# Kernel optimization log

Hardware: AMD Instinct MI355X
Metric: run time of the kernel (lower is better)

## Reference

```python
import jax, jax.numpy as jnp
import numpy as np

B, T, E, H, C = 64, 256, 1024, 1024, 32000


def setup_inputs() -> dict:
    key = jax.random.key(0)
    ks = jax.random.split(key, 8)
    s = 0.02
    return {
        "X": jax.random.randint(ks[0], (B, T), 0, C),
        "emb": jax.random.normal(ks[1], (C, E), jnp.float32) * s,
        "Wi1": jax.random.normal(ks[2], (4, H, E), jnp.float32) * s,
        "Wh1": jax.random.normal(ks[3], (4, H, H), jnp.float32) * s,
        "bi1": jnp.ones((4, H), jnp.float32),
        "bh1": jnp.ones((4, H), jnp.float32),
        "Wi2": jax.random.normal(ks[4], (4, H, E), jnp.float32) * s,
        "Wh2": jax.random.normal(ks[5], (4, H, H), jnp.float32) * s,
        "bi2": jnp.ones((4, H), jnp.float32),
        "bh2": jnp.ones((4, H), jnp.float32),
        "W": jax.random.normal(ks[6], (C, H), jnp.float32) * s,
        "b": jnp.ones((C,), jnp.float32),
    }


def _lstm_last_o(x_tbe, Wi, Wh, bi, bh):
    """Run LSTM over time; return the LAST output gate o_T, shape [B, H].

    x_tbe: [T, B, E]; Wi: [4, H, E]; Wh: [4, H, H]; bi, bh: [4, H]
    Gate order g = 0:i, 1:f, 2:g(cell cand), 3:o. Original module adds BOTH
    biases (b_i_* + b_h_*) every step.
    """
    Tn, Bn = x_tbe.shape[0], x_tbe.shape[1]
    Hn = Wh.shape[1]
    # Precompute input projections for all timesteps: [T, B, 4, H]
    xp = jnp.einsum('tbe,ghe->tbgh', x_tbe, Wi) + bi + bh

    def step(carry, xp_t):
        h, c, _ = carry
        g = xp_t + jnp.einsum('bh,gkh->bgk', h, Wh)  # [B, 4, H]
        i_t = jax.nn.sigmoid(g[:, 0])
        f_t = jax.nn.sigmoid(g[:, 1])
        g_t = jnp.tanh(g[:, 2])
        o_t = jax.nn.sigmoid(g[:, 3])
        c_new = f_t * c + i_t * g_t
        h_new = o_t * jnp.tanh(c_new)
        return (h_new, c_new, o_t), None

    z = jnp.zeros((Bn, Hn), x_tbe.dtype)
    (h_f, c_f, o_f), _ = jax.lax.scan(step, (z, z, z), xp)
    return o_f


def reference(X, emb, Wi1, Wh1, bi1, bh1, Wi2, Wh2, bi2, bh2, W, b):
    x = emb[X]                     # [B, T, E]
    xt = jnp.transpose(x, (1, 0, 2))  # [T, B, E]
    o1 = _lstm_last_o(xt, Wi1, Wh1, bi1, bh1)           # forward direction
    o2 = _lstm_last_o(xt[::-1], Wi2, Wh2, bi2, bh2)     # reversed direction
    return (o1 + o2) @ W.T + b      # [B, n_class]
```

## Files before the change

### kernel.cpp

```cpp
#include <hip/hip_runtime.h>
#include <hip/hip_bf16.h>
#include <stdint.h>

typedef __attribute__((ext_vector_type(4))) float    f32x4;
typedef __attribute__((ext_vector_type(8))) short    bf16x8;
typedef __attribute__((ext_vector_type(4))) uint32_t u32x4;
typedef unsigned short u16;

#define T_   256
#define B_   64
#define E_   1024
#define H_   1024
#define CLS  32000
#define NWG  256

#define OFF_XBF   0ull
#define OFF_WHP   33554432ull
#define OFF_FLG   67108864ull
#define OFF_BSUM  67141632ull
#define OFF_OBUF  67174400ull
#define OFF_OSUM  67698688ull
#define OFF_HROT  67829760ull

__device__ __forceinline__ u16 f2bf(float f) {
    union { float f; uint32_t i; } v; v.f = f;
    uint32_t r = v.i + 0x7fffu + ((v.i >> 16) & 1u);
    return (u16)(r >> 16);
}
__device__ __forceinline__ float sigm(float x)   { return 1.f / (1.f + __expf(-x)); }
__device__ __forceinline__ float tanh_f(float x) { return 1.f - 2.f / (__expf(2.f * x) + 1.f); }

__device__ __forceinline__ void ldg4_cc(unsigned& d, const unsigned* p) {
    asm volatile("global_load_dword %0, %1, off sc0 sc1"
                 : "=v"(d) : "v"(p) : "memory");
}
__device__ __forceinline__ void stg16_cc(u16* p, bf16x8 v) {
    asm volatile("global_store_dwordx4 %0, %1, off sc0 sc1"
                 :: "v"(p), "v"(v) : "memory");
}
__device__ __forceinline__ void stg4_cc(unsigned* p, unsigned v) {
    asm volatile("global_store_dword %0, %1, off sc0 sc1"
                 :: "v"(p), "v"(v) : "memory");
}
__device__ __forceinline__ void wait_vm0() {
    asm volatile("s_waitcnt vmcnt(0)" ::: "memory");
}


__global__ void k_gather(const int* __restrict__ X, const float* __restrict__ emb,
                         u16* __restrict__ xbf) {
    const int m = blockIdx.x;
    const int t = m >> 6, b = m & 63;
    const int tok = X[b * T_ + t];
    const float* src = emb + (size_t)tok * E_;
    u16* dst = xbf + (size_t)m * E_;
    const int e = threadIdx.x * 4;
    float4 v = *(const float4*)(src + e);
    ushort4 o; o.x = f2bf(v.x); o.y = f2bf(v.y); o.z = f2bf(v.z); o.w = f2bf(v.w);
    *(ushort4*)(dst + e) = o;
}

__global__ void k_packw(const float* __restrict__ Wi1, const float* __restrict__ Wh1,
                        const float* __restrict__ Wi2, const float* __restrict__ Wh2,
                        u16* __restrict__ whp) {
    const int gi  = blockIdx.x * 256 + threadIdx.x;
    const int half = gi >> 20;
    const int r   = gi & 1048575;
    const int wg  = r >> 12;
    const int lin = r & 4095;
    const int kc  = lin & 127;
    const int col = lin >> 7;
    const int dir = wg >> 7, hblk = wg & 127;
    const int g = col >> 3, hh = col & 7;
    const float* W = half ? (dir ? Wh2 : Wh1) : (dir ? Wi2 : Wi1);
    const float* src = W + (size_t)(g * H_ + hblk * 8 + hh) * H_ + kc * 8;
    float4 v0 = *(const float4*)(src);
    float4 v1 = *(const float4*)(src + 4);
    const uint32_t boff = (uint32_t)(((kc * 32 + col) * 16) ^ ((kc & 3) << 4));
    u16* dst = whp + (size_t)wg * 65536 + half * 32768 + boff / 2;
    ushort4 o0, o1;
    o0.x = f2bf(v0.x); o0.y = f2bf(v0.y); o0.z = f2bf(v0.z); o0.w = f2bf(v0.w);
    o1.x = f2bf(v1.x); o1.y = f2bf(v1.y); o1.z = f2bf(v1.z); o1.w = f2bf(v1.w);
    *(ushort4*)dst = o0;
    *(ushort4*)(dst + 4) = o1;
}

__global__ void k_bias(const float* __restrict__ bi1, const float* __restrict__ bh1,
                       const float* __restrict__ bi2, const float* __restrict__ bh2,
                       float* __restrict__ bsum) {
    const int i = blockIdx.x * 256 + threadIdx.x;
    bsum[i] = (i < 4096) ? (bi1[i] + bh1[i]) : (bi2[i - 4096] + bh2[i - 4096]);
}

__global__ __launch_bounds__(512, 1) void k_lstm(
    const u16* __restrict__ xbf, const u16* __restrict__ whp,
    const float* __restrict__ bsum, u16* hrot,
    float* __restrict__ obuf, unsigned* cnt) {
    __shared__ __align__(16) u16 wlds[65536];
    __shared__ float glds[2][64][35];
    __shared__ __align__(16) u16 hxch[64][8];
    const int wg = blockIdx.x;
    const int dir = wg >> 7, hblk = wg & 127;
    const int tid = threadIdx.x;
    const int wid = tid >> 6, lane = tid & 63;
    const int mtile = wid & 3, khalf = wid >> 2;
    const int col16 = lane & 15, kslot = lane >> 4;
    {
        const u32x4* s = (const u32x4*)(whp + (size_t)wg * 65536);
        u32x4* d = (u32x4*)wlds;
#pragma unroll
        for (int i = 0; i < 16; ++i) d[tid + i * 512] = s[tid + i * 512];
    }
    const int fb = tid >> 3, fh = tid & 7;
    const int hidx = hblk * 8 + fh;
    const int arow = mtile * 16 + col16;
    float bsF[4];
#pragma unroll
    for (int g = 0; g < 4; ++g) bsF[g] = bsum[dir * 4096 + g * 1024 + hidx];
    const unsigned* pollp = cnt + (size_t)(dir * 128 + khalf * 64 + lane) * 32;
    unsigned* flag_own = cnt + (size_t)(dir * 128 + hblk) * 32;
    float cc = 0.f;
    __syncthreads();
    for (int s = 0; s < T_; ++s) {
        const int t = dir ? (T_ - 1 - s) : s;
        const u16* xrow = xbf + (size_t)(t * 64 + arow) * 1024 + khalf * 512;
        bf16x8 xa[16];
#pragma unroll
        for (int kk = 0; kk < 16; ++kk)
            xa[kk] = *(const bf16x8*)(xrow + kk * 32 + kslot * 8);
        if (s > 0) {
            const unsigned target = (unsigned)s;
            for (;;) {
                unsigned f;
                ldg4_cc(f, pollp);
                wait_vm0();
                if (__all(f >= target)) break;
                __builtin_amdgcn_s_sleep(1);
            }
        }
        __builtin_amdgcn_sched_barrier(0);
        const u16* hbase = hrot + (size_t)(s * 2 + dir) * 131072
                         + (size_t)(khalf * 64) * 512 + arow * 8;
        bf16x8 hf[16];
#pragma unroll
        for (int kk = 0; kk < 16; ++kk)
            hf[kk] = *(const bf16x8*)(hbase + (size_t)(kk * 4 + kslot) * 512);
        f32x4 acc0 = {0.f, 0.f, 0.f, 0.f}, acc1 = {0.f, 0.f, 0.f, 0.f};
#pragma unroll
        for (int kk = 0; kk < 16; ++kk) {
            const int kc = khalf * 64 + kk * 4 + kslot;
            const uint32_t base = (uint32_t)(kc * 512);
            const uint32_t sw = (uint32_t)((kc & 3) << 4);
            bf16x8 b0 = *(const bf16x8*)((const char*)wlds + ((base + (uint32_t)(col16 * 16)) ^ sw));
            bf16x8 b1 = *(const bf16x8*)((const char*)wlds + ((base + (uint32_t)(256 + col16 * 16)) ^ sw));
            acc0 = __builtin_amdgcn_mfma_f32_16x16x32_bf16(xa[kk], b0, acc0, 0, 0, 0);
            acc1 = __builtin_amdgcn_mfma_f32_16x16x32_bf16(xa[kk], b1, acc1, 0, 0, 0);
        }
#pragma unroll
        for (int kk = 0; kk < 16; ++kk) {
            const int kc = khalf * 64 + kk * 4 + kslot;
            const uint32_t base = (uint32_t)(65536 + kc * 512);
            const uint32_t sw = (uint32_t)((kc & 3) << 4);
            bf16x8 b0 = *(const bf16x8*)((const char*)wlds + ((base + (uint32_t)(col16 * 16)) ^ sw));
            bf16x8 b1 = *(const bf16x8*)((const char*)wlds + ((base + (uint32_t)(256 + col16 * 16)) ^ sw));
            acc0 = __builtin_amdgcn_mfma_f32_16x16x32_bf16(hf[kk], b0, acc0, 0, 0, 0);
            acc1 = __builtin_amdgcn_mfma_f32_16x16x32_bf16(hf[kk], b1, acc1, 0, 0, 0);
        }
#pragma unroll
        for (int q = 0; q < 4; ++q) {
            glds[khalf][mtile * 16 + kslot * 4 + q][col16]      = acc0[q];
            glds[khalf][mtile * 16 + kslot * 4 + q][16 + col16] = acc1[q];
        }
        __syncthreads();
        const float gi = glds[0][fb][fh]      + glds[1][fb][fh]      + bsF[0];
        const float gf = glds[0][fb][8 + fh]  + glds[1][fb][8 + fh]  + bsF[1];
        const float gc = glds[0][fb][16 + fh] + glds[1][fb][16 + fh] + bsF[2];
        const float go = glds[0][fb][24 + fh] + glds[1][fb][24 + fh] + bsF[3];
        const float iv = sigm(gi), fv = sigm(gf), gv = tanh_f(gc), ov = sigm(go);
        cc = fv * cc + iv * gv;
        const float hv = ov * tanh_f(cc);
        hxch[fb][fh] = f2bf(hv);
        if (s == T_ - 1) obuf[(size_t)(dir * 64 + fb) * 1024 + hidx] = ov;
        __syncthreads();
        if (wid == 0) {
            bf16x8 hv8 = *(const bf16x8*)(&hxch[lane][0]);
            u16* hst = hrot + (size_t)((s + 1) * 2 + dir) * 131072
                     + (size_t)hblk * 512 + lane * 8;
            stg16_cc(hst, hv8);
            wait_vm0();
            if (lane == 0) stg4_cc(flag_own, (unsigned)(s + 1));
        }
    }
}


__global__ void k_osum(const float* __restrict__ obuf, u16* __restrict__ osum) {
    const int i = blockIdx.x * 256 + threadIdx.x;
    osum[i] = f2bf(obuf[i] + obuf[65536 + i]);
}

__global__ __launch_bounds__(256) void k_cls(const u16* __restrict__ osum,
                                             const float* __restrict__ W,
                                             const float* __restrict__ bias,
                                             float* __restrict__ out) {
    const int blk = blockIdx.x;
    const int tid = threadIdx.x, wid = tid >> 6, lane = tid & 63;
    const int col16 = lane & 15, kslot = lane >> 4;
    const int ncol0 = blk * 128 + wid * 32;
    f32x4 acc[4][2] = {};
    for (int kk = 0; kk < 32; ++kk) {
        const int kof = kk * 32 + kslot * 8;
        bf16x8 a[4];
#pragma unroll
        for (int mi = 0; mi < 4; ++mi)
            a[mi] = *(const bf16x8*)(osum + (mi * 16 + col16) * 1024 + kof);
#pragma unroll
        for (int nt = 0; nt < 2; ++nt) {
            const float* wr = W + (size_t)(ncol0 + nt * 16 + col16) * 1024 + kof;
            float4 w0 = *(const float4*)wr;
            float4 w1 = *(const float4*)(wr + 4);
            union { bf16x8 v; u16 u[8]; } bb;
            bb.u[0] = f2bf(w0.x); bb.u[1] = f2bf(w0.y); bb.u[2] = f2bf(w0.z); bb.u[3] = f2bf(w0.w);
            bb.u[4] = f2bf(w1.x); bb.u[5] = f2bf(w1.y); bb.u[6] = f2bf(w1.z); bb.u[7] = f2bf(w1.w);
#pragma unroll
            for (int mi = 0; mi < 4; ++mi)
                acc[mi][nt] = __builtin_amdgcn_mfma_f32_16x16x32_bf16(a[mi], bb.v, acc[mi][nt], 0, 0, 0);
        }
    }
#pragma unroll
    for (int nt = 0; nt < 2; ++nt) {
        const int cn = ncol0 + nt * 16 + col16;
        const float bv = bias[cn];
#pragma unroll
        for (int mi = 0; mi < 4; ++mi)
#pragma unroll
            for (int q = 0; q < 4; ++q)
                out[(size_t)(mi * 16 + kslot * 4 + q) * CLS + cn] = acc[mi][nt][q] + bv;
    }
}


extern "C" void kernel_launch(void* const* d_in, const int* in_sizes, int n_in,
                              void* d_out, int out_size, void* d_ws, size_t ws_size,
                              hipStream_t stream) {
    const int*   X   = (const int*)d_in[0];
    const float* emb = (const float*)d_in[1];
    const float* Wi1 = (const float*)d_in[2];
    const float* Wh1 = (const float*)d_in[3];
    const float* bi1 = (const float*)d_in[4];
    const float* bh1 = (const float*)d_in[5];
    const float* Wi2 = (const float*)d_in[6];
    const float* Wh2 = (const float*)d_in[7];
    const float* bi2 = (const float*)d_in[8];
    const float* bh2 = (const float*)d_in[9];
    const float* W   = (const float*)d_in[10];
    const float* bb  = (const float*)d_in[11];
    float* out = (float*)d_out;
    char* ws = (char*)d_ws;

    u16*      xbf   = (u16*)(ws + OFF_XBF);
    u16*      whp   = (u16*)(ws + OFF_WHP);
    unsigned* cnt   = (unsigned*)(ws + OFF_FLG);
    float*    bsum  = (float*)(ws + OFF_BSUM);
    float*    obuf  = (float*)(ws + OFF_OBUF);
    u16*      osum  = (u16*)(ws + OFF_OSUM);
    u16*      hrot  = (u16*)(ws + OFF_HROT);

    k_gather<<<dim3(16384), dim3(256), 0, stream>>>(X, emb, xbf);
    k_packw<<<dim3(8192), dim3(256), 0, stream>>>(Wi1, Wh1, Wi2, Wh2, whp);
    k_bias<<<dim3(32), dim3(256), 0, stream>>>(bi1, bh1, bi2, bh2, bsum);
    hipMemsetAsync(hrot, 0, 262144, stream);
    hipMemsetAsync(cnt, 0, 32768, stream);
    {
        const u16* xb_p = xbf; const u16* whp_p = whp; const float* bs_p = bsum;
        u16* hr_p = hrot; float* ob_p = obuf; unsigned* cnt_p = cnt;
        void* args[] = { (void*)&xb_p, (void*)&whp_p, (void*)&bs_p,
                         (void*)&hr_p, (void*)&ob_p, (void*)&cnt_p };
        hipError_t e = hipLaunchCooperativeKernel((void*)k_lstm, dim3(NWG), dim3(512),
                                                  args, 0, stream);
        if (e != hipSuccess) {
            k_lstm<<<dim3(NWG), dim3(512), 0, stream>>>(xbf, whp, bsum, hrot, obuf, cnt);
        }
    }
    k_osum<<<dim3(256), dim3(256), 0, stream>>>(obuf, osum);
    k_cls<<<dim3(250), dim3(256), 0, stream>>>(osum, W, bb, out);
    (void)in_sizes; (void)n_in; (void)out_size; (void)ws_size;
}
```

Before: 1.753 ms.

## Split waves into input-projection and recurrent groups to overlap x GEMM with flag wait

Instead of each wave group doing half of both the input projection and the recurrent h GEMM after the barrier, waves 0-3 now compute the full x·Wi contribution, which needs no synchronization, while waves 4-7 poll the flags and compute the full h·Wh contribution. This takes the x-projection work off the serial critical path between timesteps. The cost is that the recurrent half now runs twice as many MFMAs per wave after the flag wait, so the critical path may lengthen if that GEMM dominates. The h-publishing wave is moved to wave 4 so it belongs to the recurrent group.

```diff
diff --git a/kernel.cpp b/kernel.cpp
--- a/kernel.cpp
+++ b/kernel.cpp
@@ -103,7 +103,7 @@
     const int dir = wg >> 7, hblk = wg & 127;
     const int tid = threadIdx.x;
     const int wid = tid >> 6, lane = tid & 63;
-    const int mtile = wid & 3, khalf = wid >> 2;
+    const int mtile = wid & 3, part = wid >> 2;
     const int col16 = lane & 15, kslot = lane >> 4;
     {
         const u32x4* s = (const u32x4*)(whp + (size_t)wg * 65536);
@@ -117,59 +117,70 @@
     float bsF[4];
 #pragma unroll
     for (int g = 0; g < 4; ++g) bsF[g] = bsum[dir * 4096 + g * 1024 + hidx];
-    const unsigned* pollp = cnt + (size_t)(dir * 128 + khalf * 64 + lane) * 32;
+    const unsigned* poll0 = cnt + (size_t)(dir * 128 + lane) * 32;
+    const unsigned* poll1 = cnt + (size_t)(dir * 128 + 64 + lane) * 32;
     unsigned* flag_own = cnt + (size_t)(dir * 128 + hblk) * 32;
     float cc = 0.f;
     __syncthreads();
     for (int s = 0; s < T_; ++s) {
-        const int t = dir ? (T_ - 1 - s) : s;
-        const u16* xrow = xbf + (size_t)(t * 64 + arow) * 1024 + khalf * 512;
-        bf16x8 xa[16];
-#pragma unroll
-        for (int kk = 0; kk < 16; ++kk)
-            xa[kk] = *(const bf16x8*)(xrow + kk * 32 + kslot * 8);
-        if (s > 0) {
-            const unsigned target = (unsigned)s;
-            for (;;) {
-                unsigned f;
-                ldg4_cc(f, pollp);
-                wait_vm0();
-                if (__all(f >= target)) break;
-                __builtin_amdgcn_s_sleep(1);
-            }
-        }
-        __builtin_amdgcn_sched_barrier(0);
-        const u16* hbase = hrot + (size_t)(s * 2 + dir) * 131072
-                         + (size_t)(khalf * 64) * 512 + arow * 8;
-        bf16x8 hf[16];
-#pragma unroll
-        for (int kk = 0; kk < 16; ++kk)
-            hf[kk] = *(const bf16x8*)(hbase + (size_t)(kk * 4 + kslot) * 512);
         f32x4 acc0 = {0.f, 0.f, 0.f, 0.f}, acc1 = {0.f, 0.f, 0.f, 0.f};
-#pragma unroll
-        for (int kk = 0; kk < 16; ++kk) {
-            const int kc = khalf * 64 + kk * 4 + kslot;
-            const uint32_t base = (uint32_t)(kc * 512);
-            const uint32_t sw = (uint32_t)((kc & 3) << 4);
-            bf16x8 b0 = *(const bf16x8*)((const char*)wlds + ((base + (uint32_t)(col16 * 16)) ^ sw));
-            bf16x8 b1 = *(const bf16x8*)((const char*)wlds + ((base + (uint32_t)(256 + col16 * 16)) ^ sw));
-            acc0 = __builtin_amdgcn_mfma_f32_16x16x32_bf16(xa[kk], b0, acc0, 0, 0, 0);
-            acc1 = __builtin_amdgcn_mfma_f32_16x16x32_bf16(xa[kk], b1, acc1, 0, 0, 0);
-        }
-#pragma unroll
-        for (int kk = 0; kk < 16; ++kk) {
-            const int kc = khalf * 64 + kk * 4 + kslot;
-            const uint32_t base = (uint32_t)(65536 + kc * 512);
-            const uint32_t sw = (uint32_t)((kc & 3) << 4);
-            bf16x8 b0 = *(const bf16x8*)((const char*)wlds + ((base + (uint32_t)(col16 * 16)) ^ sw));
-            bf16x8 b1 = *(const bf16x8*)((const char*)wlds + ((base + (uint32_t)(256 + col16 * 16)) ^ sw));
-            acc0 = __builtin_amdgcn_mfma_f32_16x16x32_bf16(hf[kk], b0, acc0, 0, 0, 0);
-            acc1 = __builtin_amdgcn_mfma_f32_16x16x32_bf16(hf[kk], b1, acc1, 0, 0, 0);
-        }
-#pragma unroll
-        for (int q = 0; q < 4; ++q) {
-            glds[khalf][mtile * 16 + kslot * 4 + q][col16]      = acc0[q];
-            glds[khalf][mtile * 16 + kslot * 4 + q][16 + col16] = acc1[q];
+        if (part == 0) {
+            const int t = dir ? (T_ - 1 - s) : s;
+            const u16* xrow = xbf + (size_t)(t * 64 + arow) * 1024;
+#pragma unroll
+            for (int kk = 0; kk < 32; ++kk) {
+                bf16x8 a = *(const bf16x8*)(xrow + kk * 32 + kslot * 8);
+                const int kc = kk * 4 + kslot;
+                const uint32_t base = (uint32_t)(kc * 512);
+                const uint32_t sw = (uint32_t)((kc & 3) << 4);
+                bf16x8 b0 = *(const bf16x8*)((const char*)wlds + ((base + (uint32_t)(col16 * 16)) ^ sw));
+                bf16x8 b1 = *(const bf16x8*)((const char*)wlds + ((base + (uint32_t)(256 + col16 * 16)) ^ sw));
+                acc0 = __builtin_amdgcn_mfma_f32_16x16x32_bf16(a, b0, acc0, 0, 0, 0);
+                acc1 = __builtin_amdgcn_mfma_f32_16x16x32_bf16(a, b1, acc1, 0, 0, 0);
+            }
+#pragma unroll
+            for (int q = 0; q < 4; ++q) {
+                glds[0][mtile * 16 + kslot * 4 + q][col16]      = acc0[q];
+                glds[0][mtile * 16 + kslot * 4 + q][16 + col16] = acc1[q];
+            }
+        } else {
+            if (s > 0) {
+                const unsigned target = (unsigned)s;
+                for (;;) {
+                    unsigned f0, f1;
+                    ldg4_cc(f0, poll0);
+                    ldg4_cc(f1, poll1);
+                    wait_vm0();
+                    if (__all(f0 >= target && f1 >= target)) break;
+                    __builtin_amdgcn_s_sleep(1);
+                }
+            }
+            __builtin_amdgcn_sched_barrier(0);
+            const u16* hbase = hrot + (size_t)(s * 2 + dir) * 131072;
+            bf16x8 hf[16];
+#pragma unroll
+            for (int half = 0; half < 2; ++half) {
+#pragma unroll
+                for (int kk = 0; kk < 16; ++kk) {
+                    const int kc = (half * 16 + kk) * 4 + kslot;
+                    hf[kk] = *(const bf16x8*)(hbase + (size_t)kc * 512 + arow * 8);
+                }
+#pragma unroll
+                for (int kk = 0; kk < 16; ++kk) {
+                    const int kc = (half * 16 + kk) * 4 + kslot;
+                    const uint32_t base = (uint32_t)(65536 + kc * 512);
+                    const uint32_t sw = (uint32_t)((kc & 3) << 4);
+                    bf16x8 b0 = *(const bf16x8*)((const char*)wlds + ((base + (uint32_t)(col16 * 16)) ^ sw));
+                    bf16x8 b1 = *(const bf16x8*)((const char*)wlds + ((base + (uint32_t)(256 + col16 * 16)) ^ sw));
+                    acc0 = __builtin_amdgcn_mfma_f32_16x16x32_bf16(hf[kk], b0, acc0, 0, 0, 0);
+                    acc1 = __builtin_amdgcn_mfma_f32_16x16x32_bf16(hf[kk], b1, acc1, 0, 0, 0);
+                }
+            }
+#pragma unroll
+            for (int q = 0; q < 4; ++q) {
+                glds[1][mtile * 16 + kslot * 4 + q][col16]      = acc0[q];
+                glds[1][mtile * 16 + kslot * 4 + q][16 + col16] = acc1[q];
+            }
         }
         __syncthreads();
         const float gi = glds[0][fb][fh]      + glds[1][fb][fh]      + bsF[0];
@@ -182,7 +193,7 @@
         hxch[fb][fh] = f2bf(hv);
         if (s == T_ - 1) obuf[(size_t)(dir * 64 + fb) * 1024 + hidx] = ov;
         __syncthreads();
-        if (wid == 0) {
+        if (wid == 4) {
             bf16x8 hv8 = *(const bf16x8*)(&hxch[lane][0]);
             u16* hst = hrot + (size_t)((s + 1) * 2 + dir) * 131072
                      + (size_t)hblk * 512 + lane * 8;
```

Result: slower. 2.136 ms (+21.8%).
